# Optimization experiments

Hardware: AMD Instinct MI355X
Metric: run time of the kernel (lower is better)

Reference implementation:

```python
import jax, jax.numpy as jnp
import numpy as np

B = 16384        # batch size
D = 128          # embedding dim == ln_bot[-1]
N_EMB = 26       # number of sparse tables
VOCAB = 50000    # rows per table
LN_BOT = [13, 512, 256, 128]
LN_TOP = [479, 1024, 1024, 512, 1]
# triangular indices matching: li=[i for i in range(ni) for j in range(i)] (offset=0, no self-interaction)
LI, LJ = np.tril_indices(N_EMB + 1, -1)


def _init_linear(key, n_in, n_out):
    kw, kb = jax.random.split(key)
    lim = 1.0 / np.sqrt(n_in)
    W = jax.random.uniform(kw, (n_in, n_out), minval=-lim, maxval=lim, dtype=jnp.float32)
    b = jax.random.uniform(kb, (n_out,), minval=-lim, maxval=lim, dtype=jnp.float32)
    return W, b


def setup_inputs() -> dict:
    key = jax.random.key(0)
    ks = jax.random.split(key, 3 + len(LN_BOT) - 1 + len(LN_TOP) - 1)
    inp = {
        "dense_x": jax.random.normal(ks[0], (B, LN_BOT[0]), dtype=jnp.float32),
        "indices": jax.random.randint(ks[1], (N_EMB, B), 0, VOCAB),
        "emb_tables": jax.random.normal(ks[2], (N_EMB, VOCAB, D), dtype=jnp.float32) * 0.01,
    }
    k = 3
    for i in range(len(LN_BOT) - 1):
        W, b = _init_linear(ks[k], LN_BOT[i], LN_BOT[i + 1]); k += 1
        inp[f"bot_W{i}"], inp[f"bot_b{i}"] = W, b
    for i in range(len(LN_TOP) - 1):
        W, b = _init_linear(ks[k], LN_TOP[i], LN_TOP[i + 1]); k += 1
        inp[f"top_W{i}"], inp[f"top_b{i}"] = W, b
    return inp


def reference(dense_x, indices, emb_tables,
              bot_W0, bot_b0, bot_W1, bot_b1, bot_W2, bot_b2,
              top_W0, top_b0, top_W1, top_b1, top_W2, top_b2, top_W3, top_b3):
    # bottom MLP (sigmoid_bot=-1 -> all ReLU)
    x = dense_x
    for W, b in ((bot_W0, bot_b0), (bot_W1, bot_b1), (bot_W2, bot_b2)):
        x = jax.nn.relu(x @ W + b)                      # [B, 128]

    # embedding lookups (bag size 1 per table)
    emb = jax.vmap(lambda t, i: t[i])(emb_tables, indices)   # [26, B, D]
    emb = jnp.transpose(emb, (1, 0, 2))                      # [B, 26, D]

    # dot interaction
    T = jnp.concatenate([x[:, None, :], emb], axis=1)        # [B, 27, D]
    Z = jnp.einsum('bid,bjd->bij', T, T)                     # [B, 27, 27]
    Zflat = Z[:, LI, LJ]                                     # [B, 351]
    R = jnp.concatenate([x, Zflat], axis=1)                  # [B, 479]

    # top MLP (sigmoid on last layer, sigmoid_top=3)
    h = R
    for W, b in ((top_W0, top_b0), (top_W1, top_b1), (top_W2, top_b2)):
        h = jax.nn.relu(h @ W + b)
    p = jax.nn.sigmoid(h @ top_W3 + top_b3)                  # [B, 1]
    return jnp.clip(p, 0.0, 1.0)                             # loss_threshold = 0.0
```

## Files before the change

kernel.cpp:

```cpp
#include <hip/hip_runtime.h>

typedef __attribute__((ext_vector_type(8))) short short8;
typedef __attribute__((ext_vector_type(4))) float f32x4;
typedef __attribute__((ext_vector_type(16))) float f32x16;

#define B_ROWS 16384

__device__ __forceinline__ float bf2f(ushort u){ return __uint_as_float(((uint)u)<<16); }
__device__ __forceinline__ ushort f2bf(float f){
  uint u = __float_as_uint(f);
  u = u + 0x7FFFu + ((u>>16)&1u);
  return (ushort)(u>>16);
}
__device__ __forceinline__ void gload_lds16(const void* g, void* l){
  __builtin_amdgcn_global_load_lds((const __attribute__((address_space(1))) unsigned*)g,
                                   (__attribute__((address_space(3))) unsigned*)l, 16, 0, 0);
}

struct TArgs { const float* in; ushort* out; int K, N, Kp; };
struct TArgs5 { TArgs a[5]; };

__global__ __launch_bounds__(256) void transp_tiled(TArgs5 args)
{
  TArgs t = args.a[blockIdx.z];
  int k0 = blockIdx.x*32, n0 = blockIdx.y*32;
  if (k0 >= t.Kp || n0 >= t.N) return;
  __shared__ float tile[32][33];
  const int c = threadIdx.x & 31, r8 = threadIdx.x >> 5;
  #pragma unroll
  for (int p=0;p<4;p++){
    int k = k0 + r8 + p*8;
    tile[r8+p*8][c] = (k < t.K) ? t.in[(size_t)k*t.N + n0 + c] : 0.f;
  }
  __syncthreads();
  #pragma unroll
  for (int p=0;p<4;p++){
    int n = n0 + r8 + p*8;
    t.out[(size_t)n*t.Kp + k0 + c] = f2bf(tile[c][r8+p*8]);
  }
}

__global__ __launch_bounds__(256) void transp_vec(const float* __restrict__ in, ushort* __restrict__ out, int n)
{
  int i = blockIdx.x*256 + threadIdx.x;
  if (i < n) out[i] = f2bf(in[i]);
}

__global__ __launch_bounds__(256) void bot0(const float* __restrict__ x, const float* __restrict__ W,
                                            const float* __restrict__ bias, ushort* __restrict__ out)
{
  int i = blockIdx.x*256 + threadIdx.x;
  int b = i>>9, n = i&511;
  const float* xr = x + (size_t)b*13;
  float s = bias[n];
  #pragma unroll
  for (int k=0;k<13;k++) s += xr[k]*W[k*512+n];
  out[i] = f2bf(fmaxf(s,0.f));
}

template<bool RELU>
__global__ __launch_bounds__(256) void gemm_bt(const ushort* __restrict__ A,
    const ushort* __restrict__ Bt, const float* __restrict__ bias,
    ushort* __restrict__ C, int M, int N, int K, int ldc)
{
  constexpr int BK=64;
  __shared__ __align__(16) ushort lA[2][128*BK];
  __shared__ __align__(16) ushort lB[2][128*BK];
  const int tid = threadIdx.x;
  const int wave = tid>>6, lane = tid&63;
  const int bm = blockIdx.x*128, bn = blockIdx.y*128;
  const int wrr = (wave>>1)*64, wcc = (wave&1)*64;
  const int lr = lane&15, lg = lane>>4;
  const int nt = K>>6;
  const int ob0 = wave*4096 + lane*16;

  f32x4 acc[4][4];
  #pragma unroll
  for (int m=0;m<4;m++)
    #pragma unroll
    for (int n=0;n<4;n++)
      #pragma unroll
      for (int j=0;j<4;j++) acc[m][n][j] = 0.f;

  auto stage = [&](int buf, int kt){
    #pragma unroll
    for (int c=0;c<4;c++){
      int o = ob0 + c*1024;
      int row = o>>7, colb = o&127;
      gload_lds16((const char*)A  + (((size_t)(bm+row)*K + (kt<<6))<<1) + colb, (char*)lA[buf] + o);
      gload_lds16((const char*)Bt + (((size_t)(bn+row)*K + (kt<<6))<<1) + colb, (char*)lB[buf] + o);
    }
  };

  stage(0, 0);
  int cur = 0;
  for (int t=0; t<nt; ++t){
    int nx = (t+1 < nt) ? t+1 : 0;
    stage(cur^1, nx);
    asm volatile("s_waitcnt vmcnt(8)" ::: "memory");
    __builtin_amdgcn_s_barrier();
    asm volatile("" ::: "memory");
    #pragma unroll
    for (int kk=0;kk<BK;kk+=32){
      short8 af[4], bfr[4];
      const int lk = kk + lg*8;
      #pragma unroll
      for (int m=0;m<4;m++) af[m]  = *(const short8*)&lA[cur][(wrr+m*16+lr)*BK + lk];
      #pragma unroll
      for (int n=0;n<4;n++) bfr[n] = *(const short8*)&lB[cur][(wcc+n*16+lr)*BK + lk];
      #pragma unroll
      for (int m=0;m<4;m++)
        #pragma unroll
        for (int n=0;n<4;n++)
          acc[m][n] = __builtin_amdgcn_mfma_f32_16x16x32_bf16(af[m], bfr[n], acc[m][n], 0,0,0);
    }
    asm volatile("" ::: "memory");
    __builtin_amdgcn_s_barrier();
    cur ^= 1;
  }

  #pragma unroll
  for (int n=0;n<4;n++){
    int col = bn + wcc + n*16 + lr;
    float bv = bias[col];
    #pragma unroll
    for (int m=0;m<4;m++){
      #pragma unroll
      for (int j=0;j<4;j++){
        int row = bm + wrr + m*16 + lg*4 + j;
        float v = acc[m][n][j] + bv;
        if (RELU) v = fmaxf(v,0.f);
        C[(size_t)row*ldc + col] = f2bf(v);
      }
    }
  }
}

template<int BN>
__global__ __launch_bounds__(512, 2) void gemm256(const ushort* __restrict__ A,
    const ushort* __restrict__ Bt, const float* __restrict__ bias,
    ushort* __restrict__ C, int K, int ldc)
{
  constexpr int  NF = BN/64;
  constexpr int  LB = BN/128;
  constexpr uint BR = (uint)BN*32u;
  constexpr uint BUFSZ = 16384u + 2u*BR;
  __shared__ __align__(16) ushort lds[2*BUFSZ];

  const int tid = threadIdx.x;
  const int wave = tid>>6, lane = tid&63;
  const uint wm = (uint)(wave>>2), wn = (uint)(wave&3);
  const uint lr = (uint)(lane&15), lg = (uint)((lane>>4)&3);
  const int bm = blockIdx.x*256, bn = blockIdx.y*BN;
  const int nt = K>>6, niter = nt>>1;

  f32x4 acc[8][NF];
  #pragma unroll
  for (int m=0;m<8;m++)
    #pragma unroll
    for (int n=0;n<NF;n++)
      #pragma unroll
      for (int j=0;j<4;j++) acc[m][n][j] = 0.f;

  short8 af[4];
  short8 bf[NF];

#define STAGE(MAT, KH, TILE, SBUF) do{                                          \
    int kt_ = (TILE);                                                           \
    int ktc_ = (kt_ < nt) ? kt_ : 0;       \
    const ushort* gb_ = (MAT) ? Bt : A;                                         \
    const uint ro_ = (MAT) ? (uint)bn : (uint)bm;                               \
    const uint rb_ = (uint)(SBUF)*BUFSZ + ((MAT) ? (16384u + (uint)(KH)*BR)     \
                                                 : ((uint)(KH)*8192u));         \
    const int nl_ = (MAT) ? LB : 2;                                             \
    _Pragma("unroll")                                                           \
    for (int j_=0; j_<nl_; ++j_){                                               \
      uint lin_ = (uint)tid*16u + (uint)j_*8192u;                               \
      uint src_ = lin_ ^ (((lin_>>7)&3u)<<4);                                   \
      uint row_ = src_>>6, colb_ = src_&63u;                                    \
      const char* g_ = (const char*)gb_ +                                       \
        (((size_t)(ro_+row_)*(size_t)K + (size_t)ktc_*64 + (KH)*32)<<1) + colb_;\
      gload_lds16(g_, (char*)lds + (size_t)rb_*2 + lin_);                       \
    }                                                                           \
  }while(0)

#define PHASE(CBUF, KKH, MH, BLOAD, SMAT, SKH, STILE, SBUF, CKPT) do{           \
    const uint ab_ = (uint)(CBUF)*BUFSZ + (uint)(KKH)*8192u;                    \
    _Pragma("unroll")                                                           \
    for (int mf_=0; mf_<4; ++mf_){                                              \
      uint r_ = wm*128u + ((uint)(MH)*4u+(uint)mf_)*16u + lr;                   \
      uint l_ = r_*64u + lg*16u;                                                \
      af[mf_] = *(const short8*)((const char*)lds + (size_t)ab_*2               \
                                 + (l_ ^ (((l_>>7)&3u)<<4)));                   \
    }                                                                           \
    if (BLOAD){                                                                 \
      const uint bb_ = (uint)(CBUF)*BUFSZ + 16384u + (uint)(KKH)*BR;            \
      _Pragma("unroll")                                                         \
      for (int nf_=0; nf_<NF; ++nf_){                                           \
        uint r_ = wn*(uint)(BN/4) + (uint)nf_*16u + lr;                         \
        uint l_ = r_*64u + lg*16u;                                              \
        bf[nf_] = *(const short8*)((const char*)lds + (size_t)bb_*2             \
                                   + (l_ ^ (((l_>>7)&3u)<<4)));                 \
      }                                                                         \
    }                                                                           \
    STAGE(SMAT, SKH, STILE, SBUF);                                              \
    asm volatile("" ::: "memory");                                              \
    __builtin_amdgcn_s_barrier();                                               \
    asm volatile("" ::: "memory");                                              \
    __builtin_amdgcn_s_setprio(1);                                              \
    _Pragma("unroll")                                                           \
    for (int mf_=0; mf_<4; ++mf_)                                               \
      _Pragma("unroll")                                                         \
      for (int nf_=0; nf_<NF; ++nf_)                                            \
        acc[(MH)*4+mf_][nf_] = __builtin_amdgcn_mfma_f32_16x16x32_bf16(         \
            af[mf_], bf[nf_], acc[(MH)*4+mf_][nf_], 0,0,0);                     \
    __builtin_amdgcn_s_setprio(0);                                              \
    if (CKPT){                                                                  \
      if constexpr (LB==2) asm volatile("s_waitcnt vmcnt(4)" ::: "memory");     \
      else                 asm volatile("s_waitcnt vmcnt(3)" ::: "memory");     \
    }                                                                           \
    asm volatile("" ::: "memory");                                              \
    __builtin_amdgcn_s_barrier();                                               \
  }while(0)

  STAGE(0,0,0,0); STAGE(1,0,0,0); STAGE(0,1,0,0); STAGE(1,1,0,0);
  STAGE(0,0,1,1); STAGE(1,0,1,1);
  if constexpr (LB==2) asm volatile("s_waitcnt vmcnt(4)" ::: "memory");
  else                 asm volatile("s_waitcnt vmcnt(3)" ::: "memory");
  asm volatile("" ::: "memory");
  __builtin_amdgcn_s_barrier();

  for (int i=0; i<niter; ++i){
    const int O  = 2*i+1;
    const int E2 = 2*i+2;
    const int O2 = 2*i+3;
    PHASE(0,0,0,true , 0,1,O ,1, false);
    PHASE(0,0,1,false, 1,1,O ,1, true );
    PHASE(0,1,0,true , 0,0,E2,0, false);
    PHASE(0,1,1,false, 1,0,E2,0, true );
    PHASE(1,0,0,true , 0,1,E2,0, false);
    PHASE(1,0,1,false, 1,1,E2,0, true );
    PHASE(1,1,0,true , 0,0,O2,1, false);
    PHASE(1,1,1,false, 1,0,O2,1, true );
  }
#undef PHASE
#undef STAGE

  #pragma unroll
  for (int nf=0; nf<NF; ++nf){
    int col = bn + (int)wn*(BN/4) + nf*16 + (int)lr;
    float bv = bias[col];
    #pragma unroll
    for (int mf=0; mf<8; ++mf){
      #pragma unroll
      for (int jj=0; jj<4; ++jj){
        int row = bm + (int)wm*128 + mf*16 + (int)lg*4 + jj;
        float v = acc[mf][nf][jj] + bv;
        C[(size_t)row*ldc + col] = f2bf(fmaxf(v, 0.f));
      }
    }
  }
}

__global__ __launch_bounds__(256) void interact(const int* __restrict__ idx,
    const float* __restrict__ emb, ushort* __restrict__ R)
{
  __shared__ __align__(16) ushort Tl[4][32][136];
  const int w = threadIdx.x>>6, l = threadIdx.x&63;
  const int b = blockIdx.x*4 + w;
  ushort* Rrow = R + (size_t)b*512;

  uint xv = ((const uint*)Rrow)[l];
  *(uint*)&Tl[w][0][2*l] = xv;

  int myidx = (l<26) ? idx[(size_t)l*B_ROWS + b] : 0;
  const int half = l>>5, lc = l&31;
  #pragma unroll
  for (int i=0;i<13;i++){
    const int row = 2*i + 1 + half;
    int e = __shfl(myidx, row - 1);
    const float4* rp = (const float4*)(emb + ((size_t)(row-1)*50000 + (size_t)e)*128);
    float4 v = rp[lc];
    uint2 pk;
    pk.x = (uint)f2bf(v.x) | ((uint)f2bf(v.y)<<16);
    pk.y = (uint)f2bf(v.z) | ((uint)f2bf(v.w)<<16);
    *(uint2*)&Tl[w][row][4*lc] = pk;
  }
  __syncthreads();

  f32x16 acc;
  #pragma unroll
  for (int i=0;i<16;i++) acc[i] = 0.f;
  #pragma unroll
  for (int kk=0;kk<8;kk++){
    short8 fa = *(const short8*)((const char*)&Tl[w][0][0] + (size_t)(l&31)*272 + kk*32 + (l>>5)*16);
    acc = __builtin_amdgcn_mfma_f32_32x32x16_bf16(fa, fa, acc, 0,0,0);
  }

  const int c = l&31;
  #pragma unroll
  for (int j=0;j<16;j++){
    int r = (j&3) + 8*(j>>2) + 4*(l>>5);
    if (c < r && r <= 26) Rrow[128 + r*(r-1)/2 + c] = f2bf(acc[j]);
  }
  if (l < 33) Rrow[479 + l] = 0;
}

__global__ __launch_bounds__(256) void finlayer(const ushort* __restrict__ h3,
    const ushort* __restrict__ wt, const float* __restrict__ b3, float* __restrict__ out)
{
  int w = threadIdx.x>>6, l = threadIdx.x&63;
  int b = blockIdx.x*4 + w;
  short8 hv = *(const short8*)(h3 + (size_t)b*512 + l*8);
  short8 wv = *(const short8*)(wt + l*8);
  float s = 0.f;
  #pragma unroll
  for (int j=0;j<8;j++) s += bf2f((ushort)hv[j])*bf2f((ushort)wv[j]);
  #pragma unroll
  for (int off=32; off>0; off>>=1) s += __shfl_xor(s, off);
  if (l==0){
    float h = s + b3[0];
    float p = 1.f/(1.f + expf(-h));
    out[b] = fminf(fmaxf(p, 0.f), 1.f);
  }
}

extern "C" void kernel_launch(void* const* d_in, const int* in_sizes, int n_in,
                              void* d_out, int out_size, void* d_ws, size_t ws_size,
                              hipStream_t stream)
{
  const float* dense_x = (const float*)d_in[0];
  const int*   indices = (const int*)d_in[1];
  const float* emb     = (const float*)d_in[2];
  const float* bW0 = (const float*)d_in[3];  const float* bb0 = (const float*)d_in[4];
  const float* bW1 = (const float*)d_in[5];  const float* bb1 = (const float*)d_in[6];
  const float* bW2 = (const float*)d_in[7];  const float* bb2 = (const float*)d_in[8];
  const float* tW0 = (const float*)d_in[9];  const float* tb0 = (const float*)d_in[10];
  const float* tW1 = (const float*)d_in[11]; const float* tb1 = (const float*)d_in[12];
  const float* tW2 = (const float*)d_in[13]; const float* tb2 = (const float*)d_in[14];
  const float* tW3 = (const float*)d_in[15]; const float* tb3 = (const float*)d_in[16];
  float* out = (float*)d_out;
  const int Bn = B_ROWS;

  char* ws = (char*)d_ws;
  size_t o = 0;
  auto alloc = [&](size_t bytes)->char*{ char* r = ws + o; o += (bytes + 255) & ~(size_t)255; return r; };
  ushort* wtB1 = (ushort*)alloc(256*512*2);
  ushort* wtB2 = (ushort*)alloc(128*256*2);
  ushort* wtT0 = (ushort*)alloc(1024*512*2);
  ushort* wtT1 = (ushort*)alloc((size_t)1024*1024*2);
  ushort* wtT2 = (ushort*)alloc(512*1024*2);
  ushort* wtT3 = (ushort*)alloc(512*2);
  ushort* P    = (ushort*)alloc((size_t)Bn*512*2);
  ushort* act1 = (ushort*)alloc((size_t)Bn*256*2);
  ushort* h1   = (ushort*)alloc((size_t)Bn*1024*2);
  ushort* h2   = (ushort*)alloc((size_t)Bn*1024*2);
  (void)ws_size; (void)in_sizes; (void)n_in; (void)out_size;

  TArgs5 ta;
  ta.a[0] = { bW1, wtB1, 512 , 256 , 512  };
  ta.a[1] = { bW2, wtB2, 256 , 128 , 256  };
  ta.a[2] = { tW0, wtT0, 479 , 1024, 512  };
  ta.a[3] = { tW1, wtT1, 1024, 1024, 1024 };
  ta.a[4] = { tW2, wtT2, 1024, 512 , 1024 };
  transp_tiled<<<dim3(32,32,5),256,0,stream>>>(ta);
  transp_vec<<<2,256,0,stream>>>(tW3, wtT3, 512);

  bot0<<<Bn*512/256,256,0,stream>>>(dense_x, bW0, bb0, P);
  gemm_bt<true><<<dim3(128,2),256,0,stream>>>(P,    wtB1, bb1, act1, Bn,256,512, 256);
  gemm_bt<true><<<dim3(128,1),256,0,stream>>>(act1, wtB2, bb2, P,    Bn,128,256, 512);

  interact<<<Bn/4,256,0,stream>>>(indices, emb, P);

  gemm256<256><<<dim3(64,4),512,0,stream>>>(P,  wtT0, tb0, h1, 512 , 1024);
  gemm256<256><<<dim3(64,4),512,0,stream>>>(h1, wtT1, tb1, h2, 1024, 1024);
  gemm256<128><<<dim3(64,4),512,0,stream>>>(h2, wtT2, tb2, P,  1024, 512);
  finlayer<<<Bn/4,256,0,stream>>>(P, wtT3, tb3, out);
}
```

Before: 201.6 us.

## Use 32x32x16 MFMA in top GEMMs, merge weight transposes, smaller tiles for narrow GEMM

The large top-MLP GEMM kernel switches from 16x16x32 to 32x32x16 bf16 MFMA instructions, reorganising fragment loads and the accumulator layout so each wave issues fewer, larger matrix ops and reads fewer LDS fragments per FLOP. The small last-layer weight conversion is folded into the tiled transpose launch as an extra z-slice, removing one kernel launch. The bottom-MLP GEMM gains a templated M-tile so the N=128 layer uses 64-row blocks and launches twice as many workgroups. These are separate ideas, and the epilogue row mapping must match the 32x32 MFMA output layout exactly.

```diff
diff --git a/kernel.cpp b/kernel.cpp
--- a/kernel.cpp
+++ b/kernel.cpp
@@ -18,11 +18,16 @@
 }
 
 struct TArgs { const float* in; ushort* out; int K, N, Kp; };
-struct TArgs5 { TArgs a[5]; };
-
-__global__ __launch_bounds__(256) void transp_tiled(TArgs5 args)
+struct TArgs6 { TArgs a[6]; };
+
+__global__ __launch_bounds__(256) void transp_tiled(TArgs6 args)
 {
   TArgs t = args.a[blockIdx.z];
+  if (t.K == 0){
+    if (blockIdx.x==0 && blockIdx.y==0)
+      for (int i = threadIdx.x; i < t.N; i += 256) t.out[i] = f2bf(t.in[i]);
+    return;
+  }
   int k0 = blockIdx.x*32, n0 = blockIdx.y*32;
   if (k0 >= t.Kp || n0 >= t.N) return;
   __shared__ float tile[32][33];
@@ -40,12 +45,6 @@
   }
 }
 
-__global__ __launch_bounds__(256) void transp_vec(const float* __restrict__ in, ushort* __restrict__ out, int n)
-{
-  int i = blockIdx.x*256 + threadIdx.x;
-  if (i < n) out[i] = f2bf(in[i]);
-}
-
 __global__ __launch_bounds__(256) void bot0(const float* __restrict__ x, const float* __restrict__ W,
                                             const float* __restrict__ bias, ushort* __restrict__ out)
 {
@@ -58,25 +57,26 @@
   out[i] = f2bf(fmaxf(s,0.f));
 }
 
-template<bool RELU>
+template<int TM, bool RELU>
 __global__ __launch_bounds__(256) void gemm_bt(const ushort* __restrict__ A,
     const ushort* __restrict__ Bt, const float* __restrict__ bias,
     ushort* __restrict__ C, int M, int N, int K, int ldc)
 {
-  constexpr int BK=64;
-  __shared__ __align__(16) ushort lA[2][128*BK];
-  __shared__ __align__(16) ushort lB[2][128*BK];
+  constexpr int BM = TM*32;
+  __shared__ __align__(16) ushort lA[2][BM*64];
+  __shared__ __align__(16) ushort lB[2][128*64];
   const int tid = threadIdx.x;
   const int wave = tid>>6, lane = tid&63;
-  const int bm = blockIdx.x*128, bn = blockIdx.y*128;
-  const int wrr = (wave>>1)*64, wcc = (wave&1)*64;
+  const int bm = blockIdx.x*BM, bn = blockIdx.y*128;
+  const int wrr = (wave>>1)*(BM/2), wcc = (wave&1)*64;
   const int lr = lane&15, lg = lane>>4;
   const int nt = K>>6;
-  const int ob0 = wave*4096 + lane*16;
-
-  f32x4 acc[4][4];
-  #pragma unroll
-  for (int m=0;m<4;m++)
+  const int obA = wave*(TM*1024) + lane*16;
+  const int obB = wave*4096 + lane*16;
+
+  f32x4 acc[TM][4];
+  #pragma unroll
+  for (int m=0;m<TM;m++)
     #pragma unroll
     for (int n=0;n<4;n++)
       #pragma unroll
@@ -84,10 +84,15 @@
 
   auto stage = [&](int buf, int kt){
     #pragma unroll
-    for (int c=0;c<4;c++){
-      int o = ob0 + c*1024;
+    for (int c=0;c<TM;c++){
+      int o = obA + c*1024;
       int row = o>>7, colb = o&127;
       gload_lds16((const char*)A  + (((size_t)(bm+row)*K + (kt<<6))<<1) + colb, (char*)lA[buf] + o);
+    }
+    #pragma unroll
+    for (int c=0;c<4;c++){
+      int o = obB + c*1024;
+      int row = o>>7, colb = o&127;
       gload_lds16((const char*)Bt + (((size_t)(bn+row)*K + (kt<<6))<<1) + colb, (char*)lB[buf] + o);
     }
   };
@@ -97,19 +102,20 @@
   for (int t=0; t<nt; ++t){
     int nx = (t+1 < nt) ? t+1 : 0;
     stage(cur^1, nx);
-    asm volatile("s_waitcnt vmcnt(8)" ::: "memory");
+    if constexpr (TM==4) asm volatile("s_waitcnt vmcnt(8)" ::: "memory");
+    else                 asm volatile("s_waitcnt vmcnt(6)" ::: "memory");
     __builtin_amdgcn_s_barrier();
     asm volatile("" ::: "memory");
     #pragma unroll
-    for (int kk=0;kk<BK;kk+=32){
-      short8 af[4], bfr[4];
+    for (int kk=0;kk<64;kk+=32){
+      short8 af[TM], bfr[4];
       const int lk = kk + lg*8;
       #pragma unroll
-      for (int m=0;m<4;m++) af[m]  = *(const short8*)&lA[cur][(wrr+m*16+lr)*BK + lk];
-      #pragma unroll
-      for (int n=0;n<4;n++) bfr[n] = *(const short8*)&lB[cur][(wcc+n*16+lr)*BK + lk];
-      #pragma unroll
-      for (int m=0;m<4;m++)
+      for (int m=0;m<TM;m++) af[m]  = *(const short8*)&lA[cur][(wrr+m*16+lr)*64 + lk];
+      #pragma unroll
+      for (int n=0;n<4;n++) bfr[n] = *(const short8*)&lB[cur][(wcc+n*16+lr)*64 + lk];
+      #pragma unroll
+      for (int m=0;m<TM;m++)
         #pragma unroll
         for (int n=0;n<4;n++)
           acc[m][n] = __builtin_amdgcn_mfma_f32_16x16x32_bf16(af[m], bfr[n], acc[m][n], 0,0,0);
@@ -124,7 +130,7 @@
     int col = bn + wcc + n*16 + lr;
     float bv = bias[col];
     #pragma unroll
-    for (int m=0;m<4;m++){
+    for (int m=0;m<TM;m++){
       #pragma unroll
       for (int j=0;j<4;j++){
         int row = bm + wrr + m*16 + lg*4 + j;
@@ -141,7 +147,7 @@
     const ushort* __restrict__ Bt, const float* __restrict__ bias,
     ushort* __restrict__ C, int K, int ldc)
 {
-  constexpr int  NF = BN/64;
+  constexpr int  NF = BN/128;
   constexpr int  LB = BN/128;
   constexpr uint BR = (uint)BN*32u;
   constexpr uint BUFSZ = 16384u + 2u*BR;
@@ -150,20 +156,19 @@
   const int tid = threadIdx.x;
   const int wave = tid>>6, lane = tid&63;
   const uint wm = (uint)(wave>>2), wn = (uint)(wave&3);
-  const uint lr = (uint)(lane&15), lg = (uint)((lane>>4)&3);
+  const uint lc = (uint)(lane&31), hi = (uint)(lane>>5);
   const int bm = blockIdx.x*256, bn = blockIdx.y*BN;
   const int nt = K>>6, niter = nt>>1;
 
-  f32x4 acc[8][NF];
-  #pragma unroll
-  for (int m=0;m<8;m++)
+  f32x16 acc[4][NF];
+  #pragma unroll
+  for (int m=0;m<4;m++)
     #pragma unroll
     for (int n=0;n<NF;n++)
       #pragma unroll
-      for (int j=0;j<4;j++) acc[m][n][j] = 0.f;
-
-  short8 af[4];
-  short8 bf[NF];
+      for (int j=0;j<16;j++) acc[m][n][j] = 0.f;
+
+  short8 bfr[2][NF];
 
 #define STAGE(MAT, KH, TILE, SBUF) do{                                          \
     int kt_ = (TILE);                                                           \
@@ -186,21 +191,28 @@
 
 #define PHASE(CBUF, KKH, MH, BLOAD, SMAT, SKH, STILE, SBUF, CKPT) do{           \
     const uint ab_ = (uint)(CBUF)*BUFSZ + (uint)(KKH)*8192u;                    \
+    short8 af_[2][2];                                                           \
     _Pragma("unroll")                                                           \
-    for (int mf_=0; mf_<4; ++mf_){                                              \
-      uint r_ = wm*128u + ((uint)(MH)*4u+(uint)mf_)*16u + lr;                   \
-      uint l_ = r_*64u + lg*16u;                                                \
-      af[mf_] = *(const short8*)((const char*)lds + (size_t)ab_*2               \
-                                 + (l_ ^ (((l_>>7)&3u)<<4)));                   \
+    for (int mfl_=0; mfl_<2; ++mfl_){                                           \
+      uint r_ = wm*128u + ((uint)(MH)*2u+(uint)mfl_)*32u + lc;                  \
+      _Pragma("unroll")                                                         \
+      for (int k2_=0; k2_<2; ++k2_){                                            \
+        uint l_ = r_*64u + hi*16u + (uint)k2_*32u;                              \
+        af_[mfl_][k2_] = *(const short8*)((const char*)lds + (size_t)ab_*2      \
+                                   + (l_ ^ (((l_>>7)&3u)<<4)));                 \
+      }                                                                         \
     }                                                                           \
     if (BLOAD){                                                                 \
       const uint bb_ = (uint)(CBUF)*BUFSZ + 16384u + (uint)(KKH)*BR;            \
       _Pragma("unroll")                                                         \
       for (int nf_=0; nf_<NF; ++nf_){                                           \
-        uint r_ = wn*(uint)(BN/4) + (uint)nf_*16u + lr;                         \
-        uint l_ = r_*64u + lg*16u;                                              \
-        bf[nf_] = *(const short8*)((const char*)lds + (size_t)bb_*2             \
-                                   + (l_ ^ (((l_>>7)&3u)<<4)));                 \
+        uint r_ = wn*(uint)(BN/4) + (uint)nf_*32u + lc;                         \
+        _Pragma("unroll")                                                       \
+        for (int k2_=0; k2_<2; ++k2_){                                          \
+          uint l_ = r_*64u + hi*16u + (uint)k2_*32u;                            \
+          bfr[k2_][nf_] = *(const short8*)((const char*)lds + (size_t)bb_*2     \
+                                     + (l_ ^ (((l_>>7)&3u)<<4)));               \
+        }                                                                       \
       }                                                                         \
     }                                                                           \
     STAGE(SMAT, SKH, STILE, SBUF);                                              \
@@ -209,11 +221,13 @@
     asm volatile("" ::: "memory");                                              \
     __builtin_amdgcn_s_setprio(1);                                              \
     _Pragma("unroll")                                                           \
-    for (int mf_=0; mf_<4; ++mf_)                                               \
+    for (int mfl_=0; mfl_<2; ++mfl_)                                            \
       _Pragma("unroll")                                                         \
       for (int nf_=0; nf_<NF; ++nf_)                                            \
-        acc[(MH)*4+mf_][nf_] = __builtin_amdgcn_mfma_f32_16x16x32_bf16(         \
-            af[mf_], bf[nf_], acc[(MH)*4+mf_][nf_], 0,0,0);                     \
+        _Pragma("unroll")                                                       \
+        for (int k2_=0; k2_<2; ++k2_)                                           \
+          acc[(MH)*2+mfl_][nf_] = __builtin_amdgcn_mfma_f32_32x32x16_bf16(      \
+              af_[mfl_][k2_], bfr[k2_][nf_], acc[(MH)*2+mfl_][nf_], 0,0,0);     \
     __builtin_amdgcn_s_setprio(0);                                              \
     if (CKPT){                                                                  \
       if constexpr (LB==2) asm volatile("s_waitcnt vmcnt(4)" ::: "memory");     \
@@ -248,14 +262,14 @@
 
   #pragma unroll
   for (int nf=0; nf<NF; ++nf){
-    int col = bn + (int)wn*(BN/4) + nf*16 + (int)lr;
+    int col = bn + (int)wn*(BN/4) + nf*32 + (int)lc;
     float bv = bias[col];
     #pragma unroll
-    for (int mf=0; mf<8; ++mf){
-      #pragma unroll
-      for (int jj=0; jj<4; ++jj){
-        int row = bm + (int)wm*128 + mf*16 + (int)lg*4 + jj;
-        float v = acc[mf][nf][jj] + bv;
+    for (int mf=0; mf<4; ++mf){
+      #pragma unroll
+      for (int reg=0; reg<16; ++reg){
+        int row = bm + (int)wm*128 + mf*32 + (reg&3) + 8*(reg>>2) + 4*(int)hi;
+        float v = acc[mf][nf][reg] + bv;
         C[(size_t)row*ldc + col] = f2bf(fmaxf(v, 0.f));
       }
     }
@@ -357,18 +371,18 @@
   ushort* h2   = (ushort*)alloc((size_t)Bn*1024*2);
   (void)ws_size; (void)in_sizes; (void)n_in; (void)out_size;
 
-  TArgs5 ta;
+  TArgs6 ta;
   ta.a[0] = { bW1, wtB1, 512 , 256 , 512  };
   ta.a[1] = { bW2, wtB2, 256 , 128 , 256  };
   ta.a[2] = { tW0, wtT0, 479 , 1024, 512  };
   ta.a[3] = { tW1, wtT1, 1024, 1024, 1024 };
   ta.a[4] = { tW2, wtT2, 1024, 512 , 1024 };
-  transp_tiled<<<dim3(32,32,5),256,0,stream>>>(ta);
-  transp_vec<<<2,256,0,stream>>>(tW3, wtT3, 512);
+  ta.a[5] = { tW3, wtT3, 0   , 512 , 0    };
+  transp_tiled<<<dim3(32,32,6),256,0,stream>>>(ta);
 
   bot0<<<Bn*512/256,256,0,stream>>>(dense_x, bW0, bb0, P);
-  gemm_bt<true><<<dim3(128,2),256,0,stream>>>(P,    wtB1, bb1, act1, Bn,256,512, 256);
-  gemm_bt<true><<<dim3(128,1),256,0,stream>>>(act1, wtB2, bb2, P,    Bn,128,256, 512);
+  gemm_bt<4,true><<<dim3(128,2),256,0,stream>>>(P,    wtB1, bb1, act1, Bn,256,512, 256);
+  gemm_bt<2,true><<<dim3(256,1),256,0,stream>>>(act1, wtB2, bb2, P,    Bn,128,256, 512);
 
   interact<<<Bn/4,256,0,stream>>>(indices, emb, P);
 
```

Result: faster. 197.0 us (-2.3%).
